# Performance work log

Measured on AMD Instinct MI355X. Metric: run time of the kernel, lower is better.

Reference implementation:

```python
import jax, jax.numpy as jnp
import numpy as np

T = 32768
D_MODEL = 512
D_HIDDEN = 512
R_MIN, R_MAX, MAX_PHASE = 0.0, 1.0, 6.28


def setup_inputs() -> dict:
    key = jax.random.key(0)
    ks = jax.random.split(key, 9)
    # parameter init, mirroring the equinox module
    theta_log = jnp.log(MAX_PHASE * jax.random.uniform(ks[0], (D_HIDDEN,)))
    u = jax.random.uniform(ks[1], (D_HIDDEN,))
    nu_log = jnp.log(-0.5 * jnp.log(u * (R_MAX ** 2 - R_MIN ** 2) + R_MIN ** 2))
    diag_lambda = jnp.exp(-jnp.exp(nu_log) + 1j * jnp.exp(theta_log))
    gamma_log = jnp.log(jnp.sqrt(1 - jnp.abs(diag_lambda) ** 2))
    B_re = jax.random.normal(ks[2], (D_HIDDEN, D_MODEL)) / jnp.sqrt(2.0 * D_MODEL)
    B_im = jax.random.normal(ks[3], (D_HIDDEN, D_MODEL)) / jnp.sqrt(2.0 * D_MODEL)
    C_re = jax.random.normal(ks[4], (D_MODEL, D_HIDDEN)) / jnp.sqrt(1.0 * D_HIDDEN)
    C_im = jax.random.normal(ks[5], (D_MODEL, D_HIDDEN)) / jnp.sqrt(1.0 * D_HIDDEN)
    D = jax.random.normal(ks[6], (D_MODEL,))
    # forward inputs
    x = jax.random.normal(ks[7], (T, D_MODEL), dtype=jnp.float32)
    start = jax.random.randint(ks[8], (T,), 0, 2).astype(jnp.bool_)
    state = jnp.zeros((1, D_HIDDEN), dtype=jnp.float32)  # initial hidden state (real zero)
    return dict(state=state, x=x, start=start, theta_log=theta_log, nu_log=nu_log,
                gamma_log=gamma_log, B_re=B_re, B_im=B_im, C_re=C_re, C_im=C_im, D=D)


def reference(state, x, start, theta_log, nu_log, gamma_log, B_re, B_im, C_re, C_im, D):
    H = nu_log.shape[0]
    diag_lambda = jnp.exp(-jnp.exp(nu_log) + 1j * jnp.exp(theta_log))  # [H] complex
    B_norm = (B_re + 1j * B_im) * jnp.exp(gamma_log)[:, None]          # [H, M]
    C = C_re + 1j * C_im                                               # [M, H]

    Bu = x.astype(B_norm.dtype) @ B_norm.T                             # [T, H]
    Lam = jnp.broadcast_to(diag_lambda, (x.shape[0], H))               # [T, H]
    # prepend identity element carrying the initial state
    Lam = jnp.concatenate([jnp.ones((1, H), Lam.dtype), Lam])          # [T+1, H]
    Bu = jnp.concatenate([state.astype(Bu.dtype), Bu])                 # [T+1, H]
    st = jnp.concatenate([jnp.zeros((1, 1), jnp.bool_), start.reshape(-1, 1)])  # [T+1, 1]

    def combine(carry, incoming):
        prev_start, sA, sb = carry
        s0, iA, ib = incoming
        keep = jnp.logical_not(s0)        # reset-wrap: zero carry at episode starts
        A = iA * (keep * sA)
        b = iA * (keep * sb) + ib
        return (jnp.logical_or(s0, prev_start), A, b)

    _, _, xs = jax.lax.associative_scan(combine, (st, Lam, Bu))
    xs = xs[1:]                                                        # [T, H] hidden states
    outputs = jnp.einsum('th,mh->tm', xs, C).real + x * D              # [T, M]
    return (xs[None, -1], outputs)
```

## Files before the change

kernel.cpp:

```cpp
#include <hip/hip_runtime.h>
#include <hip/hip_bf16.h>
#include <stdint.h>

#define T_LEN 32768
#define DM 512
#define DH 512
#define NC 512
#define CL 64

typedef __attribute__((ext_vector_type(8))) short short8;
typedef __attribute__((ext_vector_type(4))) float f32x4;

static __device__ __forceinline__ float b2f(__hip_bfloat16 v) { return __bfloat162float(v); }
static __device__ __forceinline__ __hip_bfloat16 f2b(float v) { return __float2bfloat16(v); }

static __device__ __forceinline__ void store_out(float* p, float v) { *p = v; }
static __device__ __forceinline__ void store_out(__hip_bfloat16* p, float v) { *p = f2b(v); }

static __device__ __forceinline__ float bflo(unsigned u) { return __uint_as_float(u << 16); }
static __device__ __forceinline__ float bfhi(unsigned u) { return __uint_as_float(u & 0xffff0000u); }
static __device__ __forceinline__ unsigned packbf2(float re, float im) {
    union { __hip_bfloat16 h; unsigned short s; } a, b;
    a.h = f2b(re); b.h = f2b(im);
    return (unsigned)a.s | ((unsigned)b.s << 16);
}

static __device__ __forceinline__ void load_lds16(const unsigned short* g, unsigned short* l) {
    __builtin_amdgcn_global_load_lds(
        (const __attribute__((address_space(1))) unsigned int*)g,
        (__attribute__((address_space(3))) unsigned int*)l, 16, 0, 0);
}

static __device__ __forceinline__ int get_start(const int* start, int mode, int t) {
    return mode ? (int)((const unsigned char*)start)[t] : start[t];
}

__global__ void prep_all(const float* __restrict__ x,
                         const float* __restrict__ B_re,
                         const float* __restrict__ B_im,
                         const float* __restrict__ gamma_log,
                         const float* __restrict__ C_re,
                         const float* __restrict__ C_im,
                         const unsigned* __restrict__ startw,
                         __hip_bfloat16* __restrict__ xb,
                         __hip_bfloat16* __restrict__ B1,
                         __hip_bfloat16* __restrict__ B2,
                         int* __restrict__ smode) {
    int b = blockIdx.x;
    if (b < 16384) {
        int i = (b * 256 + threadIdx.x) * 4;
        float4 v = *(const float4*)(x + i);
        xb[i + 0] = f2b(v.x);
        xb[i + 1] = f2b(v.y);
        xb[i + 2] = f2b(v.z);
        xb[i + 3] = f2b(v.w);
    } else if (b < 18432) {
        int idx = (b - 16384) * 256 + threadIdx.x;
        int row = idx >> 9;
        int m   = idx & 511;
        int h   = row >> 1;
        float g = expf(gamma_log[h]);
        float v = (row & 1) ? B_im[(size_t)h * 512 + m] : B_re[(size_t)h * 512 + m];
        B1[idx] = f2b(v * g);
    } else if (b < 20480) {
        int idx = (b - 18432) * 256 + threadIdx.x;
        int m = idx >> 10;
        int k = idx & 1023;
        int h = k >> 1;
        float v = (k & 1) ? -C_im[(size_t)m * 512 + h]
                          :  C_re[(size_t)m * 512 + h];
        B2[idx] = f2b(v);
    } else if (threadIdx.x < 64) {
        int v = 0;
        for (int i = threadIdx.x; i < 8192; i += 64) v |= (startw[i] > 1u) ? 1 : 0;
        unsigned long long bal = __ballot(v);
        if (threadIdx.x == 0) *smode = (bal != 0ull) ? 1 : 0;
    }
}

template <int KDIM, typename OutT>
__global__ void gemm_bt(const __hip_bfloat16* __restrict__ A,
                        const __hip_bfloat16* __restrict__ B,
                        OutT* __restrict__ out, int ldc,
                        const __hip_bfloat16* __restrict__ xres,
                        const float* __restrict__ Dv) {
    __shared__ unsigned short As[128 * 64];
    __shared__ unsigned short Bs[128 * 64];
    const int lane = threadIdx.x & 63;
    const int wave = threadIdx.x >> 6;
    const int by = blockIdx.x;
    const int bx = blockIdx.y;
    const int wm = (wave >> 1) * 64;
    const int wn = (wave & 1) * 64;
    const int lrow = lane >> 3;
    const int lcol = (lane & 7) * 8;

    const unsigned short* Au = (const unsigned short*)A;
    const unsigned short* Bu = (const unsigned short*)B;

    f32x4 acc[4][4] = {};

    for (int kt = 0; kt < KDIM / 64; ++kt) {
        const int k0 = kt * 64;
#pragma unroll
        for (int j = 0; j < 4; ++j) {
            int ii = wave * 4 + j;
            int row = ii * 8 + lrow;
            load_lds16(Au + (size_t)(by * 128 + row) * KDIM + k0 + lcol, &As[ii * 512]);
            load_lds16(Bu + (size_t)(bx * 128 + row) * KDIM + k0 + lcol, &Bs[ii * 512]);
        }
        __syncthreads();
#pragma unroll
        for (int ks = 0; ks < 2; ++ks) {
            short8 af[4], bfr[4];
#pragma unroll
            for (int i = 0; i < 4; ++i) {
                af[i]  = *(const short8*)&As[(wm + i * 16 + (lane & 15)) * 64 + ks * 32 + (lane >> 4) * 8];
                bfr[i] = *(const short8*)&Bs[(wn + i * 16 + (lane & 15)) * 64 + ks * 32 + (lane >> 4) * 8];
            }
#pragma unroll
            for (int i = 0; i < 4; ++i)
#pragma unroll
                for (int j = 0; j < 4; ++j)
                    acc[i][j] = __builtin_amdgcn_mfma_f32_16x16x32_bf16(af[i], bfr[j], acc[i][j], 0, 0, 0);
        }
        __syncthreads();
    }

    const int rowq = (lane >> 4) * 4;
#pragma unroll
    for (int i = 0; i < 4; ++i) {
#pragma unroll
        for (int r = 0; r < 4; ++r) {
            int row = by * 128 + wm + i * 16 + rowq + r;
#pragma unroll
            for (int j = 0; j < 4; ++j) {
                int col = bx * 128 + wn + j * 16 + (lane & 15);
                float v = acc[i][j][r];
                if (xres) v += b2f(xres[(size_t)row * DM + col]) * Dv[col];
                store_out(&out[(size_t)row * ldc + col], v);
            }
        }
    }
}

static __device__ __forceinline__ void get_lambda(const float* nu_log,
                                                  const float* theta_log,
                                                  int h, float& lr, float& li) {
    float nu = expf(nu_log[h]);
    float th = expf(theta_log[h]);
    float mag = expf(-nu);
    lr = mag * cosf(th);
    li = mag * sinf(th);
}

__global__ void scan_phase1(const unsigned* __restrict__ Bu,
                            const int* __restrict__ start,
                            const int* __restrict__ smode,
                            const float* __restrict__ nu_log,
                            const float* __restrict__ theta_log,
                            float4* __restrict__ agg) {
    const int h = threadIdx.x;
    const int c = blockIdx.x;
    const int mode = *smode;
    float lr, li;
    get_lambda(nu_log, theta_log, h, lr, li);
    float ar = 1.f, ai = 0.f, br = 0.f, bi = 0.f;
    const int t0 = c * CL;
    for (int i0 = 0; i0 < CL; i0 += 8) {
        unsigned uu[8]; int ss[8];
#pragma unroll
        for (int k = 0; k < 8; ++k) {
            int t = t0 + i0 + k;
            uu[k] = Bu[(size_t)t * 512 + h];
            ss[k] = get_start(start, mode, t);
        }
#pragma unroll
        for (int k = 0; k < 8; ++k) {
            float s = ss[k] ? 0.f : 1.f;
            float slr = lr * s, sli = li * s;
            float bur = bflo(uu[k]), bui = bfhi(uu[k]);
            float nar = slr * ar - sli * ai;
            float nai = slr * ai + sli * ar;
            float nbr = slr * br - sli * bi + bur;
            float nbi = slr * bi + sli * br + bui;
            ar = nar; ai = nai; br = nbr; bi = nbi;
        }
    }
    agg[(size_t)c * DH + h] = make_float4(ar, ai, br, bi);
}

__global__ void scan_phase2(const float4* __restrict__ agg,
                            const float* __restrict__ state,
                            float2* __restrict__ prefix) {
    const int h = threadIdx.x;
    float hr = state[h];
    float hi = 0.f;
#pragma unroll 8
    for (int c = 0; c < NC; ++c) {
        prefix[(size_t)c * DH + h] = make_float2(hr, hi);
        float4 a = agg[(size_t)c * DH + h];
        float nr = a.x * hr - a.y * hi + a.z;
        float ni = a.x * hi + a.y * hr + a.w;
        hr = nr; hi = ni;
    }
}

__global__ void scan_phase3(unsigned* __restrict__ Bu,
                            const int* __restrict__ start,
                            const int* __restrict__ smode,
                            const float* __restrict__ nu_log,
                            const float* __restrict__ theta_log,
                            const float2* __restrict__ prefix,
                            float* __restrict__ dstate, int interleaved) {
    const int h = threadIdx.x;
    const int c = blockIdx.x;
    const int mode = *smode;
    float lr, li;
    get_lambda(nu_log, theta_log, h, lr, li);
    float2 p = prefix[(size_t)c * DH + h];
    float hr = p.x, hi = p.y;
    const int t0 = c * CL;
    for (int i0 = 0; i0 < CL; i0 += 8) {
        unsigned uu[8]; int ss[8];
#pragma unroll
        for (int k = 0; k < 8; ++k) {
            int t = t0 + i0 + k;
            uu[k] = Bu[(size_t)t * 512 + h];
            ss[k] = get_start(start, mode, t);
        }
#pragma unroll
        for (int k = 0; k < 8; ++k) {
            float s = ss[k] ? 0.f : 1.f;
            float slr = lr * s, sli = li * s;
            float bur = bflo(uu[k]), bui = bfhi(uu[k]);
            float nhr = slr * hr - sli * hi + bur;
            float nhi = slr * hi + sli * hr + bui;
            hr = nhr; hi = nhi;
            Bu[(size_t)(t0 + i0 + k) * 512 + h] = packbf2(hr, hi);
        }
    }
    if (c == NC - 1) {
        if (interleaved) {
            dstate[2 * h]     = hr;
            dstate[2 * h + 1] = hi;
        } else {
            dstate[h] = hr;
        }
    }
}

extern "C" void kernel_launch(void* const* d_in, const int* in_sizes, int n_in,
                              void* d_out, int out_size, void* d_ws, size_t ws_size,
                              hipStream_t stream) {
    const float* state = (const float*)d_in[0];
    const float* x     = (const float*)d_in[1];
    const int*   start = (const int*)d_in[2];
    const float* theta = (const float*)d_in[3];
    const float* nu    = (const float*)d_in[4];
    const float* gam   = (const float*)d_in[5];
    const float* B_re  = (const float*)d_in[6];
    const float* B_im  = (const float*)d_in[7];
    const float* C_re  = (const float*)d_in[8];
    const float* C_im  = (const float*)d_in[9];
    const float* Dv    = (const float*)d_in[10];
    float* out = (float*)d_out;

    const long long t_dm = (long long)T_LEN * DM;
    int state_floats = (int)((long long)out_size - t_dm);
    int interleaved = (state_floats >= 1024) ? 1 : 0;
    if (state_floats < 512) state_floats = 512;

    char* ws = (char*)d_ws;
    __hip_bfloat16* xb = (__hip_bfloat16*)(ws);
    __hip_bfloat16* B1 = (__hip_bfloat16*)(ws + (32ll << 20));
    __hip_bfloat16* B2 = (__hip_bfloat16*)(ws + (33ll << 20));
    __hip_bfloat16* Bu = (__hip_bfloat16*)(ws + (34ll << 20));
    float4* agg        = (float4*)(ws + (98ll << 20));
    float2* pre        = (float2*)(ws + (102ll << 20));
    int* smode         = (int*)(ws + (104ll << 20));

    prep_all<<<20481, 256, 0, stream>>>(x, B_re, B_im, gam, C_re, C_im,
                                        (const unsigned*)start, xb, B1, B2, smode);
    gemm_bt<512, __hip_bfloat16><<<dim3(256, 8), 256, 0, stream>>>(xb, B1, Bu, 1024, nullptr, nullptr);
    scan_phase1<<<NC, 512, 0, stream>>>((const unsigned*)Bu, start, smode, nu, theta, agg);
    scan_phase2<<<1, 512, 0, stream>>>(agg, state, pre);
    scan_phase3<<<NC, 512, 0, stream>>>((unsigned*)Bu, start, smode, nu, theta, pre, out, interleaved);
    gemm_bt<1024, float><<<dim3(256, 4), 256, 0, stream>>>(Bu, B2, out + state_floats, 512, xb, Dv);
}
```

Baseline: 358.7 us.

## Parallelize chunk-prefix scan across hidden dims with shared-memory Hillis-Steele scan

Replaces the single-block serial loop over 512 chunks with one block per hidden channel that performs a log-depth parallel scan in shared memory over transposed chunk aggregates. Phase 1 now writes aggregates in hidden-major layout so each block reads contiguous data. This removes a long serial dependency chain on a single CU, at the cost of strided uncoalesced writes in phase 1 and extra work in the scan.

```diff
diff --git a/kernel.cpp b/kernel.cpp
--- a/kernel.cpp
+++ b/kernel.cpp
@@ -159,7 +159,7 @@
                             const int* __restrict__ smode,
                             const float* __restrict__ nu_log,
                             const float* __restrict__ theta_log,
-                            float4* __restrict__ agg) {
+                            float4* __restrict__ aggT) {
     const int h = threadIdx.x;
     const int c = blockIdx.x;
     const int mode = *smode;
@@ -187,23 +187,38 @@
             ar = nar; ai = nai; br = nbr; bi = nbi;
         }
     }
-    agg[(size_t)c * DH + h] = make_float4(ar, ai, br, bi);
-}
-
-__global__ void scan_phase2(const float4* __restrict__ agg,
+    aggT[(size_t)h * NC + c] = make_float4(ar, ai, br, bi);
+}
+
+__global__ void scan_phase2(const float4* __restrict__ aggT,
                             const float* __restrict__ state,
                             float2* __restrict__ prefix) {
-    const int h = threadIdx.x;
-    float hr = state[h];
-    float hi = 0.f;
-#pragma unroll 8
-    for (int c = 0; c < NC; ++c) {
-        prefix[(size_t)c * DH + h] = make_float2(hr, hi);
-        float4 a = agg[(size_t)c * DH + h];
-        float nr = a.x * hr - a.y * hi + a.z;
-        float ni = a.x * hi + a.y * hr + a.w;
-        hr = nr; hi = ni;
-    }
+    __shared__ float4 s[NC];
+    const int h = blockIdx.x;
+    const int c = threadIdx.x;
+    float4 v = (c == 0) ? make_float4(1.f, 0.f, 0.f, 0.f)
+                        : aggT[(size_t)h * NC + (c - 1)];
+    s[c] = v;
+    __syncthreads();
+#pragma unroll
+    for (int off = 1; off < NC; off <<= 1) {
+        float4 left;
+        if (c >= off) left = s[c - off];
+        __syncthreads();
+        if (c >= off) {
+            float Ar = v.x * left.x - v.y * left.y;
+            float Ai = v.x * left.y + v.y * left.x;
+            float br = v.x * left.z - v.y * left.w + v.z;
+            float bi = v.x * left.w + v.y * left.z + v.w;
+            v = make_float4(Ar, Ai, br, bi);
+            s[c] = v;
+        }
+        __syncthreads();
+    }
+    float st = state[h];
+    float pr = v.x * st + v.z;
+    float pi = v.y * st + v.w;
+    prefix[(size_t)c * DH + h] = make_float2(pr, pi);
 }
 
 __global__ void scan_phase3(unsigned* __restrict__ Bu,
@@ -276,15 +291,15 @@
     __hip_bfloat16* B1 = (__hip_bfloat16*)(ws + (32ll << 20));
     __hip_bfloat16* B2 = (__hip_bfloat16*)(ws + (33ll << 20));
     __hip_bfloat16* Bu = (__hip_bfloat16*)(ws + (34ll << 20));
-    float4* agg        = (float4*)(ws + (98ll << 20));
+    float4* aggT       = (float4*)(ws + (98ll << 20));
     float2* pre        = (float2*)(ws + (102ll << 20));
     int* smode         = (int*)(ws + (104ll << 20));
 
     prep_all<<<20481, 256, 0, stream>>>(x, B_re, B_im, gam, C_re, C_im,
                                         (const unsigned*)start, xb, B1, B2, smode);
     gemm_bt<512, __hip_bfloat16><<<dim3(256, 8), 256, 0, stream>>>(xb, B1, Bu, 1024, nullptr, nullptr);
-    scan_phase1<<<NC, 512, 0, stream>>>((const unsigned*)Bu, start, smode, nu, theta, agg);
-    scan_phase2<<<1, 512, 0, stream>>>(agg, state, pre);
+    scan_phase1<<<NC, 512, 0, stream>>>((const unsigned*)Bu, start, smode, nu, theta, aggT);
+    scan_phase2<<<512, NC, 0, stream>>>(aggT, state, pre);
     scan_phase3<<<NC, 512, 0, stream>>>((unsigned*)Bu, start, smode, nu, theta, pre, out, interleaved);
     gemm_bt<1024, float><<<dim3(256, 4), 256, 0, stream>>>(Bu, B2, out + state_floats, 512, xb, Dv);
 }
```

Measured after the change: 301.5 us. 15.9% less time.
